# Kernel tuning notes

Measured on AMD Instinct MI355X. Metric: run time of the kernel, lower is better.

Reference implementation:

```python
import jax, jax.numpy as jnp
import numpy as np

VOCAB = 100000
EMB_DIM = 50
KERNEL_NUM = 21
SIGMA = 0.1
EXACT_SIGMA = 0.001

# kernel mus/sigmas exactly as KNRM._get_kernels_layers
_MUS = [(2.0 * (i + 1) - KERNEL_NUM) / (KERNEL_NUM - 1) for i in range(KERNEL_NUM - 1)] + [1.0]
_SIGMAS = [SIGMA] * (KERNEL_NUM - 1) + [EXACT_SIGMA]


def setup_inputs() -> dict:
    key = jax.random.key(0)
    k1, k2, k3, k4, k5, k6, k7 = jax.random.split(key, 7)
    B, Lq, Ld = 1024, 32, 512
    return {
        "query_1": jax.random.randint(k1, (B, Lq), 0, VOCAB),
        "document_1": jax.random.randint(k2, (B, Ld), 0, VOCAB),
        "query_2": jax.random.randint(k3, (B, Lq), 0, VOCAB),
        "document_2": jax.random.randint(k4, (B, Ld), 0, VOCAB),
        "emb": jax.random.normal(k5, (VOCAB, EMB_DIM), dtype=jnp.float32),
        "mlp_w": jax.random.normal(k6, (1, KERNEL_NUM), dtype=jnp.float32) * 0.1,
        "mlp_b": jax.random.normal(k7, (1,), dtype=jnp.float32) * 0.1,
    }


def _predict(q_idx, d_idx, emb, mlp_w, mlp_b):
    q = emb[q_idx]                                   # [B, Lq, E]
    d = emb[d_idx]                                   # [B, Ld, E]
    qn = jnp.linalg.norm(q, axis=2)                  # [B, Lq]
    dn = jnp.linalg.norm(d, axis=2)                  # [B, Ld]
    sim = jnp.einsum('bqe,bde->bqd', q, d)
    sim = sim / (qn[:, :, None] * dn[:, None, :])
    sim = jnp.where(jnp.isnan(sim), 0.0, sim)        # [B, Lq, Ld]
    KM = []
    for mu, s in zip(_MUS, _SIGMAS):
        g = jnp.exp(-(sim - mu) ** 2 / (2.0 * s * s))
        KM.append(jnp.sum(jnp.log1p(jnp.sum(g, axis=-1)), axis=-1))
    kernels_out = jnp.stack(KM, axis=1)              # [B, 21]
    return kernels_out @ mlp_w.T + mlp_b             # [B, 1]


def reference(query_1, document_1, query_2, document_2, emb, mlp_w, mlp_b):
    logits_1 = _predict(query_1, document_1, emb, mlp_w, mlp_b)
    logits_2 = _predict(query_2, document_2, emb, mlp_w, mlp_b)
    return jax.nn.sigmoid(logits_1 - logits_2)
```

## Files before the change

kernel.cpp:

```cpp
#include <hip/hip_runtime.h>
#include <math.h>

#define LOG2E 1.4426950408889634f

typedef __attribute__((ext_vector_type(8))) short    short8;
typedef __attribute__((ext_vector_type(8))) _Float16 half8;
typedef __attribute__((ext_vector_type(4))) float    f32x4;
typedef __attribute__((ext_vector_type(2))) float    f32x2;

__device__ __forceinline__ float fexp2(float x) { return __builtin_amdgcn_exp2f(x); }

typedef __attribute__((address_space(1))) const unsigned int gas_u32;
typedef __attribute__((address_space(3))) unsigned int las_u32;
__device__ __forceinline__ void glds16(const uint4* g, uint4* l)
{ __builtin_amdgcn_global_load_lds((gas_u32*)g, (las_u32*)l, 16, 0, 0); }

__device__ __forceinline__ void kern21(f32x2 s, f32x2* acc)
{
    s.x = __builtin_amdgcn_fmed3f(s.x, -1.1f, 1.1f);
    s.y = __builtin_amdgcn_fmed3f(s.y, -1.1f, 1.1f);

    f32x2 va = s * 14.426950408889634f + 0.7213475204444817f;
    f32x2 v, vi, gc;
    v.x  = fexp2(va.x);  v.y  = fexp2(va.y);
    vi.x = __builtin_amdgcn_rcpf(v.x);
    vi.y = __builtin_amdgcn_rcpf(v.y);
    f32x2 t9 = s + 0.05f;
    f32x2 ga = (t9 * t9) * -72.13475204444817f;
    gc.x = fexp2(ga.x);  gc.y = fexp2(ga.y);

    f32x2 p = gc;
    acc[9] += p;
    #pragma unroll
    for (int k = 10; k <= 19; ++k) { p *= v; acc[k] += p; }
    f32x2 q = gc;
    #pragma unroll
    for (int k = 8; k >= 0; --k) { q *= vi; acc[k] += q; }
    if (__any(fmaxf(s.x, s.y) > 0.995f)) {
        f32x2 te = s - 1.0f;
        f32x2 ea = (te * te) * -721347.5204444817f;
        f32x2 ge; ge.x = fexp2(ea.x); ge.y = fexp2(ea.y);
        acc[20] += ge;
    }
}

__device__ __forceinline__ void doc_step2(
    half8 A0, half8 A1, half8 B0, half8 B1, f32x2* acc)
{
    f32x4 C = {0.f, 0.f, 0.f, 0.f};
    C = __builtin_amdgcn_mfma_f32_16x16x32_f16(A0, B0, C, 0, 0, 0);
    C = __builtin_amdgcn_mfma_f32_16x16x32_f16(A1, B1, C, 0, 0, 0);
    f32x2 a01 = {C[0], C[1]};
    f32x2 a23 = {C[2], C[3]};
    kern21(a01, acc);
    kern21(a23, acc);
}

__global__ __launch_bounds__(256) void knrm_prep_kernel(
    const float* __restrict__ emb, uint4* __restrict__ wse, int vocab)
{
    const int tid = threadIdx.x;
    const int row = blockIdx.x * 32 + (tid >> 3);
    const int cb  = tid & 7;
    if (row >= vocab) return;

    const float* src = emb + (size_t)row * 50;
    float v[8];
    float ss = 0.f;
    #pragma unroll
    for (int p = 0; p < 4; ++p) {
        int e = cb * 8 + 2 * p;
        float2 t;
        if (e + 2 <= 50) t = *(const float2*)(src + e);
        else             t = make_float2(0.f, 0.f);
        v[2*p]   = t.x;
        v[2*p+1] = t.y;
        ss = fmaf(t.x, t.x, fmaf(t.y, t.y, ss));
    }
    ss += __shfl_xor(ss, 1, 64);
    ss += __shfl_xor(ss, 2, 64);
    ss += __shfl_xor(ss, 4, 64);
    float rn = __builtin_amdgcn_rsqf(ss);

    half8 hv;
    #pragma unroll
    for (int p = 0; p < 8; ++p) hv[p] = (_Float16)(v[p] * rn);
    wse[(size_t)row * 8 + cb] = __builtin_bit_cast(uint4, hv);
}

__device__ __forceinline__ half8 frag_ldh(const uint4* mat, int row, int chunk)
{
    return __builtin_bit_cast(half8, mat[row * 8 + (chunk ^ (row & 7))]);
}

__global__ __launch_bounds__(256, 4) void knrm_pass_pre(
    const int* __restrict__ q1, const int* __restrict__ d1,
    const int* __restrict__ q2, const int* __restrict__ d2,
    const uint4* __restrict__ wse, const float* __restrict__ mlp_w,
    float* __restrict__ ws_logit)
{
    __shared__ uint4 dbuf[4][2][256];
    __shared__ float Swk[4][21][16];
    __shared__ float wred[4];

    const int tid  = threadIdx.x;
    const int bx   = blockIdx.x;
    const int b    = bx >> 1;
    const int lane = tid & 63;
    const int wave = tid >> 6;
    const int g    = lane >> 4;

    const int* qidx = ((bx & 1) ? q2 : q1) + b * 32;
    const int* dd   = ((bx & 1) ? d2 : d1) + b * 512 + (wave & 1) * 256;

    const int qrow = (wave >> 1) * 16 + (lane & 15);
    const uint4* qb = wse + (size_t)qidx[qrow] * 8;
    half8 B0 = __builtin_bit_cast(half8, qb[g]);
    half8 B1 = __builtin_bit_cast(half8, qb[4 + g]);

    const int rsub = lane >> 3;
    const int swz  = (lane & 7) ^ rsub;

    uint4* buf0 = dbuf[wave][0];
    uint4* buf1 = dbuf[wave][1];

    int t0 = dd[rsub], t1 = dd[8 + rsub], t2 = dd[16 + rsub], t3 = dd[24 + rsub];
    glds16(wse + (size_t)t0 * 8 + swz, buf0);
    glds16(wse + (size_t)t1 * 8 + swz, buf0 + 64);
    glds16(wse + (size_t)t2 * 8 + swz, buf0 + 128);
    glds16(wse + (size_t)t3 * 8 + swz, buf0 + 192);
    t0 = dd[32 + rsub]; t1 = dd[40 + rsub]; t2 = dd[48 + rsub]; t3 = dd[56 + rsub];

    f32x2 acc2[21];
    #pragma unroll
    for (int k = 0; k < 21; ++k) acc2[k] = (f32x2){0.f, 0.f};

    const int ar0 = lane & 15;
    const int ar1 = 16 + ar0;

    for (int c = 0; c < 8; ++c) {
        asm volatile("s_waitcnt vmcnt(0)" ::: "memory");
        __builtin_amdgcn_sched_barrier(0);

        uint4* cur = (c & 1) ? buf1 : buf0;
        uint4* nxt = (c & 1) ? buf0 : buf1;

        if (c < 7) {
            glds16(wse + (size_t)t0 * 8 + swz, nxt);
            glds16(wse + (size_t)t1 * 8 + swz, nxt + 64);
            glds16(wse + (size_t)t2 * 8 + swz, nxt + 128);
            glds16(wse + (size_t)t3 * 8 + swz, nxt + 192);
            if (c < 6) {
                t0 = dd[(c + 2) * 32 + rsub];
                t1 = dd[(c + 2) * 32 + 8 + rsub];
                t2 = dd[(c + 2) * 32 + 16 + rsub];
                t3 = dd[(c + 2) * 32 + 24 + rsub];
            }
        }

        doc_step2(frag_ldh(cur, ar0, g), frag_ldh(cur, ar0, 4 + g), B0, B1, acc2);
        doc_step2(frag_ldh(cur, ar1, g), frag_ldh(cur, ar1, 4 + g), B0, B1, acc2);
    }

    float acc[21];
    #pragma unroll
    for (int k = 0; k < 21; ++k) {
        float v = acc2[k].x + acc2[k].y;
        v += __shfl_xor(v, 16, 64);
        v += __shfl_xor(v, 32, 64);
        acc[k] = v;
    }
    if (lane < 16) {
        #pragma unroll
        for (int k = 0; k < 21; ++k) Swk[wave][k][lane] = acc[k];
    }
    __syncthreads();

    float local = 0.f;
    for (int p = tid; p < 21 * 32; p += 256) {
        int k = p >> 5, q = p & 31;
        int wp = (q >> 4) * 2;
        float S = Swk[wp][k][q & 15] + Swk[wp + 1][k][q & 15];
        float j = (float)(k - 9);
        float scale = (k < 20) ? fexp2(-0.7213475204444817f * j * j) : 1.0f;
        local += mlp_w[k] * log1pf(S * scale);
    }
    #pragma unroll
    for (int off = 1; off < 64; off <<= 1) local += __shfl_xor(local, off, 64);
    if (lane == 0) wred[wave] = local;
    __syncthreads();
    if (tid == 0)
        ws_logit[bx] = wred[0] + wred[1] + wred[2] + wred[3];
}

__device__ __forceinline__ short8 frag_ldb(const uint4* mat, int row, int chunk)
{
    return __builtin_bit_cast(short8, mat[row * 8 + (chunk ^ (row & 7))]);
}

__device__ __forceinline__ void doc_step_fb(
    short8 Ah0, short8 Ah1, short8 Al0, short8 Al1,
    short8 Bh0, short8 Bh1, short8 Bl0, short8 Bl1, f32x2* acc)
{
    f32x4 C = {0.f, 0.f, 0.f, 0.f};
    C = __builtin_amdgcn_mfma_f32_16x16x32_bf16(Ah0, Bh0, C, 0, 0, 0);
    C = __builtin_amdgcn_mfma_f32_16x16x32_bf16(Ah1, Bh1, C, 0, 0, 0);
    C = __builtin_amdgcn_mfma_f32_16x16x32_bf16(Ah0, Bl0, C, 0, 0, 0);
    C = __builtin_amdgcn_mfma_f32_16x16x32_bf16(Ah1, Bl1, C, 0, 0, 0);
    C = __builtin_amdgcn_mfma_f32_16x16x32_bf16(Al0, Bh0, C, 0, 0, 0);
    C = __builtin_amdgcn_mfma_f32_16x16x32_bf16(Al1, Bh1, C, 0, 0, 0);
    f32x2 a01 = {C[0], C[1]};
    f32x2 a23 = {C[2], C[3]};
    kern21(a01, acc);
    kern21(a23, acc);
}

__device__ __forceinline__ void stage_row_chunk(
    const float* __restrict__ emb, int tok, int row, int cb,
    uint4* __restrict__ hmat, uint4* __restrict__ lmat)
{
    const float* src = emb + (size_t)tok * 50;
    float v[8];
    float ss = 0.f;
    #pragma unroll
    for (int p = 0; p < 4; ++p) {
        int e = cb * 8 + 2 * p;
        float2 t;
        if (e + 2 <= 50) t = *(const float2*)(src + e);
        else             t = make_float2(0.f, 0.f);
        v[2*p]   = t.x;
        v[2*p+1] = t.y;
        ss = fmaf(t.x, t.x, fmaf(t.y, t.y, ss));
    }
    ss += __shfl_xor(ss, 1, 64);
    ss += __shfl_xor(ss, 2, 64);
    ss += __shfl_xor(ss, 4, 64);
    float rn = __builtin_amdgcn_rsqf(ss);

    unsigned hw[4], lw[4];
    #pragma unroll
    for (int p = 0; p < 4; ++p) {
        float a = v[2*p]   * rn;
        float b = v[2*p+1] * rn;
        unsigned ha = __float_as_uint(a) & 0xFFFF0000u;
        unsigned hb = __float_as_uint(b) & 0xFFFF0000u;
        float la = a - __uint_as_float(ha);
        float lb = b - __uint_as_float(hb);
        hw[p] = (ha >> 16) | hb;
        lw[p] = (__float_as_uint(la) >> 16) | (__float_as_uint(lb) & 0xFFFF0000u);
    }
    int cidx = cb ^ (row & 7);
    hmat[row * 8 + cidx] = make_uint4(hw[0], hw[1], hw[2], hw[3]);
    lmat[row * 8 + cidx] = make_uint4(lw[0], lw[1], lw[2], lw[3]);
}

__global__ __launch_bounds__(256, 4) void knrm_pass_fb(
    const int* __restrict__ q1, const int* __restrict__ d1,
    const int* __restrict__ q2, const int* __restrict__ d2,
    const float* __restrict__ emb, const float* __restrict__ mlp_w,
    float* __restrict__ ws_logit)
{
    __shared__ uint4 qh4[256], ql4[256];
    __shared__ uint4 dh4[256], dl4[256];
    __shared__ float Swk[4][21][16];
    __shared__ float wred[4];

    const int tid  = threadIdx.x;
    const int bx   = blockIdx.x;
    const int b    = bx >> 1;
    const int lane = tid & 63;
    const int wave = tid >> 6;
    const int g    = lane >> 4;

    const int* qidx = ((bx & 1) ? q2 : q1) + b * 32;
    const int* didx = ((bx & 1) ? d2 : d1) + b * 512;

    const int srow = tid >> 3;
    const int scb  = tid & 7;

    stage_row_chunk(emb, qidx[srow], srow, scb, qh4, ql4);
    __syncthreads();

    const int qrow = (wave >> 1) * 16 + (lane & 15);
    short8 Bh0 = frag_ldb(qh4, qrow, g);
    short8 Bh1 = frag_ldb(qh4, qrow, 4 + g);
    short8 Bl0 = frag_ldb(ql4, qrow, g);
    short8 Bl1 = frag_ldb(ql4, qrow, 4 + g);

    f32x2 acc2[21];
    #pragma unroll
    for (int k = 0; k < 21; ++k) acc2[k] = (f32x2){0.f, 0.f};

    const int arow = (wave & 1) * 16 + (lane & 15);

    for (int c = 0; c < 16; ++c) {
        if (c) __syncthreads();
        stage_row_chunk(emb, didx[c * 32 + srow], srow, scb, dh4, dl4);
        __syncthreads();
        doc_step_fb(frag_ldb(dh4, arow, g), frag_ldb(dh4, arow, 4 + g),
                    frag_ldb(dl4, arow, g), frag_ldb(dl4, arow, 4 + g),
                    Bh0, Bh1, Bl0, Bl1, acc2);
    }
    __syncthreads();

    float acc[21];
    #pragma unroll
    for (int k = 0; k < 21; ++k) {
        float v = acc2[k].x + acc2[k].y;
        v += __shfl_xor(v, 16, 64);
        v += __shfl_xor(v, 32, 64);
        acc[k] = v;
    }
    if (lane < 16) {
        #pragma unroll
        for (int k = 0; k < 21; ++k) Swk[wave][k][lane] = acc[k];
    }
    __syncthreads();

    float local = 0.f;
    for (int p = tid; p < 21 * 32; p += 256) {
        int k = p >> 5, q = p & 31;
        int wp = (q >> 4) * 2;
        float S = Swk[wp][k][q & 15] + Swk[wp + 1][k][q & 15];
        float j = (float)(k - 9);
        float scale = (k < 20) ? fexp2(-0.7213475204444817f * j * j) : 1.0f;
        local += mlp_w[k] * log1pf(S * scale);
    }
    #pragma unroll
    for (int off = 1; off < 64; off <<= 1) local += __shfl_xor(local, off, 64);
    if (lane == 0) wred[wave] = local;
    __syncthreads();
    if (tid == 0)
        ws_logit[bx] = wred[0] + wred[1] + wred[2] + wred[3];
}

__global__ void knrm_final_kernel(const float* __restrict__ P,
                                  float* __restrict__ out, int B)
{
    int i = blockIdx.x * 256 + threadIdx.x;
    if (i < B) {
        float x = P[2 * i] - P[2 * i + 1];
        out[i] = 1.0f / (1.0f + fexp2(-LOG2E * x));
    }
}

extern "C" void kernel_launch(void* const* d_in, const int* in_sizes, int n_in,
                              void* d_out, int out_size, void* d_ws, size_t ws_size,
                              hipStream_t stream) {
    const int*   q1    = (const int*)d_in[0];
    const int*   d1    = (const int*)d_in[1];
    const int*   q2    = (const int*)d_in[2];
    const int*   d2    = (const int*)d_in[3];
    const float* emb   = (const float*)d_in[4];
    const float* mlp_w = (const float*)d_in[5];
    float*       out   = (float*)d_out;

    const int B     = out_size;
    const int vocab = in_sizes[4] / 50;

    float* ws_logit = (float*)d_ws;
    uint4* wse      = (uint4*)((char*)d_ws + 8192);
    size_t need     = 8192 + (size_t)vocab * 128;

    if (ws_size >= need) {
        knrm_prep_kernel<<<dim3((vocab + 31) / 32), dim3(256), 0, stream>>>(emb, wse, vocab);
        knrm_pass_pre<<<dim3(2 * B), dim3(256), 0, stream>>>(
            q1, d1, q2, d2, wse, mlp_w, ws_logit);
    } else {
        knrm_pass_fb<<<dim3(2 * B), dim3(256), 0, stream>>>(
            q1, d1, q2, d2, emb, mlp_w, ws_logit);
    }
    knrm_final_kernel<<<dim3((B + 255) / 256), dim3(256), 0, stream>>>(ws_logit, out, B);
}
```

Before: 61.38 us.

## Software-pipeline MFMA one chunk ahead of Gaussian kernel evaluation

Result: no change. 60.69 us (-1.1%).

```diff
diff --git a/kernel.cpp b/kernel.cpp
--- a/kernel.cpp
+++ b/kernel.cpp
@@ -44,16 +44,21 @@
     }
 }
 
-__device__ __forceinline__ void doc_step2(
-    half8 A0, half8 A1, half8 B0, half8 B1, f32x2* acc)
+__device__ __forceinline__ f32x4 mfma2(half8 A0, half8 A1, half8 B0, half8 B1)
 {
     f32x4 C = {0.f, 0.f, 0.f, 0.f};
     C = __builtin_amdgcn_mfma_f32_16x16x32_f16(A0, B0, C, 0, 0, 0);
     C = __builtin_amdgcn_mfma_f32_16x16x32_f16(A1, B1, C, 0, 0, 0);
-    f32x2 a01 = {C[0], C[1]};
-    f32x2 a23 = {C[2], C[3]};
-    kern21(a01, acc);
-    kern21(a23, acc);
+    return C;
+}
+
+__device__ __forceinline__ void kern4(f32x4 C0, f32x4 C1, f32x2* acc)
+{
+    f32x2 a, b;
+    a.x = C0[0]; a.y = C0[1]; kern21(a, acc);
+    b.x = C0[2]; b.y = C0[3]; kern21(b, acc);
+    a.x = C1[0]; a.y = C1[1]; kern21(a, acc);
+    b.x = C1[2]; b.y = C1[3]; kern21(b, acc);
 }
 
 __global__ __launch_bounds__(256) void knrm_prep_kernel(
@@ -138,12 +143,30 @@
     const int ar0 = lane & 15;
     const int ar1 = 16 + ar0;
 
-    for (int c = 0; c < 8; ++c) {
+    asm volatile("s_waitcnt vmcnt(0)" ::: "memory");
+    __builtin_amdgcn_sched_barrier(0);
+    f32x4 Cp0, Cp1;
+    {
+        half8 A00 = frag_ldh(buf0, ar0, g), A01 = frag_ldh(buf0, ar0, 4 + g);
+        half8 A10 = frag_ldh(buf0, ar1, g), A11 = frag_ldh(buf0, ar1, 4 + g);
+        glds16(wse + (size_t)t0 * 8 + swz, buf1);
+        glds16(wse + (size_t)t1 * 8 + swz, buf1 + 64);
+        glds16(wse + (size_t)t2 * 8 + swz, buf1 + 128);
+        glds16(wse + (size_t)t3 * 8 + swz, buf1 + 192);
+        t0 = dd[64 + rsub]; t1 = dd[72 + rsub]; t2 = dd[80 + rsub]; t3 = dd[88 + rsub];
+        Cp0 = mfma2(A00, A01, B0, B1);
+        Cp1 = mfma2(A10, A11, B0, B1);
+    }
+
+    for (int c = 1; c < 8; ++c) {
         asm volatile("s_waitcnt vmcnt(0)" ::: "memory");
         __builtin_amdgcn_sched_barrier(0);
 
         uint4* cur = (c & 1) ? buf1 : buf0;
         uint4* nxt = (c & 1) ? buf0 : buf1;
+
+        half8 A00 = frag_ldh(cur, ar0, g), A01 = frag_ldh(cur, ar0, 4 + g);
+        half8 A10 = frag_ldh(cur, ar1, g), A11 = frag_ldh(cur, ar1, 4 + g);
 
         if (c < 7) {
             glds16(wse + (size_t)t0 * 8 + swz, nxt);
@@ -158,9 +181,13 @@
             }
         }
 
-        doc_step2(frag_ldh(cur, ar0, g), frag_ldh(cur, ar0, 4 + g), B0, B1, acc2);
-        doc_step2(frag_ldh(cur, ar1, g), frag_ldh(cur, ar1, 4 + g), B0, B1, acc2);
-    }
+        kern4(Cp0, Cp1, acc2);
+
+        __builtin_amdgcn_sched_barrier(0);
+        Cp0 = mfma2(A00, A01, B0, B1);
+        Cp1 = mfma2(A10, A11, B0, B1);
+    }
+    kern4(Cp0, Cp1, acc2);
 
     float acc[21];
     #pragma unroll
@@ -209,8 +236,8 @@
     C = __builtin_amdgcn_mfma_f32_16x16x32_bf16(Ah1, Bl1, C, 0, 0, 0);
     C = __builtin_amdgcn_mfma_f32_16x16x32_bf16(Al0, Bh0, C, 0, 0, 0);
     C = __builtin_amdgcn_mfma_f32_16x16x32_bf16(Al1, Bh1, C, 0, 0, 0);
-    f32x2 a01 = {C[0], C[1]};
-    f32x2 a23 = {C[2], C[3]};
+    f32x2 a01; a01.x = C[0]; a01.y = C[1];
+    f32x2 a23; a23.x = C[2]; a23.y = C[3];
     kern21(a01, acc);
     kern21(a23, acc);
 }
```
